# Optimization experiments

Measured on AMD Instinct MI355X. Metric: run time of the kernel, lower is better.

Reference implementation:

```python
import jax, jax.numpy as jnp
import numpy as np

B, C_IN, N, K, UP = 8, 128, 2048, 8, 4
C_MID = C_IN + 3  # 131

def _pw1(x, W):  # pointwise Conv1d: x (B,C,N), W (O,C)
    return jnp.einsum('oc,bcn->bon', W, x)

def _pw2(x, W):  # pointwise Conv2d: x (B,C,N,K), W (O,C)
    return jnp.einsum('oc,bcnk->bonk', W, x)

def _bn(x, g, b):  # eval-mode BatchNorm (running mean 0, var 1)
    shp = (1, -1) + (1,) * (x.ndim - 2)
    return x * g.reshape(shp) + b.reshape(shp)

def _gather(tab, idx):  # tab (B,S,D), idx (B,...) -> (B,...,D)
    return jax.vmap(lambda t, i: t[i])(tab, idx)

def _fps(pts, npoint):  # pts (B,n,c) -> idx (B,npoint), iterative farthest point sampling
    b, n, _ = pts.shape
    dist0 = jnp.full((b, n), 1e10, pts.dtype)
    far0 = jnp.zeros((b,), jnp.int32)
    def body(carry, _):
        dist, far = carry
        cen = jax.vmap(lambda p, i: p[i])(pts, far)[:, None, :]  # (b,1,c)
        d = jnp.sum((pts - cen) ** 2, axis=-1)
        dist = jnp.minimum(dist, d)
        return (dist, jnp.argmax(dist, axis=-1).astype(jnp.int32)), far
    (_, _), idx = jax.lax.scan(body, (dist0, far0), None, length=npoint)
    return idx.T  # (B, npoint)

def _forward(feature, input, rel_pos_emb, w_skip, g_skip, b_skip, w_m1, w_m2, g_m2, b_m2,
             w_out1, g_out1, b_out1, w_out2, g_out2, b_out2, w_q, w_k, w_v, b_v,
             w_t, b_t, g_ra, b_ra, w_mlp1, w_conv2, g_conv2, b_conv2):
    b, c, n = feature.shape
    s = n // UP
    pts = feature.reshape(b, n, c)  # mirrors torch .reshape(B,N,C)
    far = _fps(pts, s)                          # (B,S) FPS in feature space
    down_feats = _gather(pts, far)              # (B,S,C) downsampled features
    xyz = jnp.transpose(input, (0, 2, 1))       # (B,N,3)
    cand_xyz = _gather(xyz, far)                # (B,S,3)
    # kNN: each of N input points -> k nearest downsampled points (xyz space)
    d2 = (jnp.sum(xyz ** 2, -1)[:, :, None] + jnp.sum(cand_xyz ** 2, -1)[:, None, :]
          - 2.0 * jnp.einsum('bnd,bsd->bns', xyz, cand_xyz))
    _, idx = jax.lax.top_k(-d2, K)              # (B,N,K)
    gp = jnp.transpose(_gather(cand_xyz, idx), (0, 3, 1, 2))    # (B,3,N,K)
    gf = jnp.transpose(_gather(down_feats, idx), (0, 3, 1, 2))  # (B,C,N,K)
    gp = gp - input[:, :, :, None]              # relative coords
    feats = jnp.concatenate([gf, gp], axis=1)   # (B,131,N,K)
    skip = jnp.max(feats, axis=3)
    skip = jax.nn.relu(_bn(_pw1(skip, w_skip), g_skip, b_skip))         # (B,256,N)
    f = jax.nn.relu(_pw2(feats, w_m1))
    f = jax.nn.relu(_bn(_pw2(f, w_m2), g_m2, b_m2))                     # (B,256,N,K)
    # output_mlp1: Conv2d(k->256, kernel [1,256]) on f.transpose(1,3)
    g1 = jnp.einsum('okw,bwnk->bon', w_out1, f)                         # (B,256,N)
    g1 = jax.nn.relu(_bn(g1, g_out1, b_out1))
    g1 = g1 + skip
    g1 = jax.nn.relu(_bn(_pw1(g1, w_out2), g_out2, b_out2))             # (B,128,N)
    glob = jnp.concatenate([g1, input], axis=1)                          # (B,131,N)
    # RA_Layer1: PCT-style offset attention
    q = jnp.transpose(_pw1(glob, w_q), (0, 2, 1))                        # (B,N,32)
    kk = _pw1(glob, w_k)                                                 # (B,32,N)
    v = _pw1(glob, w_v) + b_v[None, :, None]
    att = jax.nn.softmax(jnp.einsum('bnc,bcm->bnm', q, kk), axis=-1)     # (B,N,N)
    att = att / (1e-9 + att.sum(axis=1, keepdims=True))
    x_r = jnp.einsum('bcm,bmn->bcn', v, att)
    x_r = jax.nn.relu(_bn(_pw1(glob - x_r, w_t) + b_t[None, :, None], g_ra, b_ra))
    ra = glob + x_r
    out = jax.nn.relu(_pw1(ra, w_mlp1))                                  # (B,256,N)
    out = jax.nn.relu(_bn(_pw1(out, w_conv2), g_conv2, b_conv2))         # (B,128,N)
    return out

def setup_inputs():
    key = jax.random.key(0)
    ks = iter(jax.random.split(key, 40))
    def nrm(shape, scale=1.0):
        return jax.random.normal(next(ks), shape, jnp.float32) * scale
    return {
        'feature': nrm((B, C_IN, N)),
        'input': nrm((B, 3, N)),
        'rel_pos_emb': nrm((B, 3, N)),
        'w_skip': nrm((256, C_MID), 0.05), 'g_skip': jnp.ones((256,)), 'b_skip': jnp.zeros((256,)),
        'w_m1': nrm((256, C_MID), 0.05),
        'w_m2': nrm((256, 256), 0.05), 'g_m2': jnp.ones((256,)), 'b_m2': jnp.zeros((256,)),
        'w_out1': nrm((256, K, 256), 0.02), 'g_out1': jnp.ones((256,)), 'b_out1': jnp.zeros((256,)),
        'w_out2': nrm((128, 256), 0.05), 'g_out2': jnp.ones((128,)), 'b_out2': jnp.zeros((128,)),
        'w_q': nrm((C_MID // 4, C_MID), 0.05), 'w_k': nrm((C_MID // 4, C_MID), 0.05),
        'w_v': nrm((C_MID, C_MID), 0.05), 'b_v': jnp.zeros((C_MID,)),
        'w_t': nrm((C_MID, C_MID), 0.05), 'b_t': jnp.zeros((C_MID,)),
        'g_ra': jnp.ones((C_MID,)), 'b_ra': jnp.zeros((C_MID,)),
        'w_mlp1': nrm((256, C_MID), 0.05),
        'w_conv2': nrm((128, 256), 0.05), 'g_conv2': jnp.ones((128,)), 'b_conv2': jnp.zeros((128,)),
    }

def reference(feature, input, rel_pos_emb, w_skip, g_skip, b_skip, w_m1, w_m2, g_m2, b_m2,
              w_out1, g_out1, b_out1, w_out2, g_out2, b_out2, w_q, w_k, w_v, b_v,
              w_t, b_t, g_ra, b_ra, w_mlp1, w_conv2, g_conv2, b_conv2):
    return _forward(feature, input, rel_pos_emb, w_skip, g_skip, b_skip, w_m1, w_m2, g_m2, b_m2,
                    w_out1, g_out1, b_out1, w_out2, g_out2, b_out2, w_q, w_k, w_v, b_v,
                    w_t, b_t, g_ra, b_ra, w_mlp1, w_conv2, g_conv2, b_conv2)
```

## Files before the change

kernel.cpp:

```cpp
#include <hip/hip_runtime.h>


#define NB 8
#define NN 2048
#define CIN 128
#define KNN 8
#define SS 512
#define CMID 131

enum { F_XT = 1, F_STORET = 4, F_XSUB = 8 };

template <int FLAGS>
__global__ __launch_bounds__(256) void gemm64_k(
    const float* __restrict__ W, size_t wbs,
    const float* __restrict__ X, size_t xbs,
    const float* __restrict__ X2,
    float* __restrict__ Y, size_t ybs, int ldyt,
    int O, int K, int M,
    const float* __restrict__ bias,
    const float* __restrict__ gamma,
    const float* __restrict__ beta,
    const float* __restrict__ skip, size_t skipbs,
    const float* __restrict__ colscale,
    int relu)
{
    constexpr int KC = 32;
    __shared__ float Wl[KC * 68];
    __shared__ float Xl[KC * 68];
    const int b  = blockIdx.z;
    const int o0 = blockIdx.y * 64, m0 = blockIdx.x * 64;
    const float* Wb  = W + (size_t)b * wbs;
    const float* Xb  = X + (size_t)b * xbs;
    const float* X2b = (FLAGS & F_XSUB) ? (X2 + (size_t)b * xbs) : nullptr;
    const int t  = threadIdx.x;
    const int to = t >> 4, tm = t & 15;
    const int o4 = to * 4, m4 = tm * 4;

    float acc[4][4];
#pragma unroll
    for (int i = 0; i < 4; ++i)
#pragma unroll
        for (int j = 0; j < 4; ++j) acc[i][j] = 0.f;

    for (int kk = 0; kk < K; kk += KC) {
#pragma unroll
        for (int r = 0; r < 8; ++r) {
            int e = t + r * 256;
            int ki = e & 31, o = e >> 5;
            int go = o0 + o, gk = kk + ki;
            Wl[ki * 68 + o] = (go < O && gk < K) ? Wb[(size_t)go * K + gk] : 0.f;
        }
        if (FLAGS & F_XT) {
#pragma unroll
            for (int r = 0; r < 8; ++r) {
                int e = t + r * 256;
                int ki = e & 31, m = e >> 5;
                int gm = m0 + m, gk = kk + ki;
                Xl[ki * 68 + m] = (gm < M && gk < K) ? Xb[(size_t)gm * K + gk] : 0.f;
            }
        } else {
#pragma unroll
            for (int r = 0; r < 2; ++r) {
                int e = t + r * 256;
                int kr = e >> 4, mc4 = (e & 15) * 4;
                int gk = kk + kr;
                float4 v = make_float4(0.f, 0.f, 0.f, 0.f);
                if (gk < K) {
                    v = *(const float4*)&Xb[(size_t)gk * M + m0 + mc4];
                    if (FLAGS & F_XSUB) {
                        float4 u = *(const float4*)&X2b[(size_t)gk * M + m0 + mc4];
                        v.x -= u.x; v.y -= u.y; v.z -= u.z; v.w -= u.w;
                    }
                }
                *(float4*)&Xl[kr * 68 + mc4] = v;
            }
        }
        __syncthreads();
#pragma unroll
        for (int k = 0; k < KC; ++k) {
            float4 w4 = *(const float4*)&Wl[k * 68 + o4];
            float4 x4 = *(const float4*)&Xl[k * 68 + m4];
            float wv[4] = {w4.x, w4.y, w4.z, w4.w};
            float xv[4] = {x4.x, x4.y, x4.z, x4.w};
#pragma unroll
            for (int i = 0; i < 4; ++i)
#pragma unroll
                for (int j = 0; j < 4; ++j)
                    acc[i][j] = fmaf(wv[i], xv[j], acc[i][j]);
        }
        __syncthreads();
    }
#pragma unroll
    for (int i = 0; i < 4; ++i) {
        int o = o0 + o4 + i;
        if (o >= O) continue;
        float bi_ = bias ? bias[o] : 0.f;
        float ga  = gamma ? gamma[o] : 1.f;
        float be  = gamma ? beta[o] : 0.f;
        float v4[4];
#pragma unroll
        for (int j = 0; j < 4; ++j) {
            int m = m0 + m4 + j;
            float v = acc[i][j] + bi_;
            v = v * ga + be;
            if (relu) v = fmaxf(v, 0.f);
            if (skip) v += skip[(size_t)b * skipbs + (size_t)o * M + m];
            if (colscale) v *= colscale[(size_t)b * M + m];
            v4[j] = v;
        }
        if (FLAGS & F_STORET) {
#pragma unroll
            for (int j = 0; j < 4; ++j)
                Y[(size_t)b * ybs + (size_t)(m0 + m4 + j) * ldyt + o] = v4[j];
        } else {
            float4 s = make_float4(v4[0], v4[1], v4[2], v4[3]);
            *(float4*)&Y[(size_t)b * ybs + (size_t)o * M + m0 + m4] = s;
        }
    }
}

__global__ __launch_bounds__(256) void fps_k(const float* __restrict__ G,
                                             int* __restrict__ far)
{
    const int b = blockIdx.x;
    const float* Gb = G + (size_t)b * NN * NN;
    const int t = threadIdx.x;
    const int pA = 4 * t, pB = 1024 + 4 * t;

    float4 dstA = make_float4(1e10f, 1e10f, 1e10f, 1e10f);
    float4 dstB = dstA;
    float4 dgA, dgB;
    dgA.x = Gb[(size_t)(pA + 0) * NN + (pA + 0)];
    dgA.y = Gb[(size_t)(pA + 1) * NN + (pA + 1)];
    dgA.z = Gb[(size_t)(pA + 2) * NN + (pA + 2)];
    dgA.w = Gb[(size_t)(pA + 3) * NN + (pA + 3)];
    dgB.x = Gb[(size_t)(pB + 0) * NN + (pB + 0)];
    dgB.y = Gb[(size_t)(pB + 1) * NN + (pB + 1)];
    dgB.z = Gb[(size_t)(pB + 2) * NN + (pB + 2)];
    dgB.w = Gb[(size_t)(pB + 3) * NN + (pB + 3)];

    __shared__ float sv[2][4];
    __shared__ int   si[2][4];
    int cur = 0;
    if (t == 0) far[b * SS] = 0;

    for (int it = 1; it < SS; ++it) {
        const float* row = Gb + (size_t)cur * NN;
        float nf = row[cur];
        float4 rA = *(const float4*)&row[pA];
        float4 rB = *(const float4*)&row[pB];

        dstA.x = fminf(dstA.x, dgA.x + nf - 2.0f * rA.x);
        dstA.y = fminf(dstA.y, dgA.y + nf - 2.0f * rA.y);
        dstA.z = fminf(dstA.z, dgA.z + nf - 2.0f * rA.z);
        dstA.w = fminf(dstA.w, dgA.w + nf - 2.0f * rA.w);
        dstB.x = fminf(dstB.x, dgB.x + nf - 2.0f * rB.x);
        dstB.y = fminf(dstB.y, dgB.y + nf - 2.0f * rB.y);
        dstB.z = fminf(dstB.z, dgB.z + nf - 2.0f * rB.z);
        dstB.w = fminf(dstB.w, dgB.w + nf - 2.0f * rB.w);

        float best = dstA.x; int bidx = pA;
        if (dstA.y > best) { best = dstA.y; bidx = pA + 1; }
        if (dstA.z > best) { best = dstA.z; bidx = pA + 2; }
        if (dstA.w > best) { best = dstA.w; bidx = pA + 3; }
        if (dstB.x > best) { best = dstB.x; bidx = pB; }
        if (dstB.y > best) { best = dstB.y; bidx = pB + 1; }
        if (dstB.z > best) { best = dstB.z; bidx = pB + 2; }
        if (dstB.w > best) { best = dstB.w; bidx = pB + 3; }

#pragma unroll
        for (int off = 32; off >= 1; off >>= 1) {
            float ov = __shfl_xor(best, off, 64);
            int   oi = __shfl_xor(bidx, off, 64);
            if (ov > best || (ov == best && oi < bidx)) { best = ov; bidx = oi; }
        }
        const int wid = t >> 6, lane = t & 63, pb = it & 1;
        if (lane == 0) { sv[pb][wid] = best; si[pb][wid] = bidx; }
        __syncthreads();
        float bb = sv[pb][0]; int bi_ = si[pb][0];
#pragma unroll
        for (int w = 1; w < 4; ++w) {
            float wv = sv[pb][w]; int wi = si[pb][w];
            if (wv > bb || (wv == bb && wi < bi_)) { bb = wv; bi_ = wi; }
        }
        cur = bi_;
        if (t == 0) far[b * SS + it] = bi_;
    }
}

__global__ __launch_bounds__(256) void gather_df_k(const float* __restrict__ feature,
                                                   const int* __restrict__ far,
                                                   float* __restrict__ dcT)
{
    int idx = blockIdx.x * 256 + threadIdx.x;
    int c = idx & 127;
    int s = (idx >> 7) & 511;
    int b = idx >> 16;
    float v = feature[(size_t)b * (NN * CIN) + (size_t)far[b * SS + s] * CIN + c];
    dcT[((size_t)b * CMID + c) * SS + s] = v;
}

__global__ void gather_cx_k(const float* __restrict__ input,
                            const int* __restrict__ far,
                            float* __restrict__ cand,
                            float* __restrict__ dcT)
{
    int idx = blockIdx.x * 64 + threadIdx.x;
    if (idx >= NB * SS) return;
    int b = idx >> 9, s = idx & 511;
    int f = far[idx];
#pragma unroll
    for (int d = 0; d < 3; ++d) {
        float v = input[((size_t)b * 3 + d) * NN + f];
        cand[idx * 3 + d] = v;
        dcT[((size_t)b * CMID + CIN + d) * SS + s] = v;
    }
}

__global__ __launch_bounds__(256) void b1_k(const float* __restrict__ W1,
                                            const float* __restrict__ input,
                                            float* __restrict__ B1)
{
    const int b = blockIdx.y;
    const int t = threadIdx.x;
    const int n = blockIdx.x * 4 + (t >> 6);
    const int w4 = (t & 63) * 4;
    float in0 = input[(size_t)b * (3 * NN) + n];
    float in1 = input[(size_t)b * (3 * NN) + NN + n];
    float in2 = input[(size_t)b * (3 * NN) + 2 * NN + n];
    float4 v;
    float* vp = &v.x;
#pragma unroll
    for (int j = 0; j < 4; ++j) {
        const float* wr = &W1[(size_t)(w4 + j) * CMID + CIN];
        vp[j] = wr[0] * in0 + wr[1] * in1 + wr[2] * in2;
    }
    *(float4*)&B1[((size_t)b * NN + n) * 256 + w4] = v;
}

__global__ __launch_bounds__(256) void w2t_k(const float* __restrict__ W2,
                                             float* __restrict__ W2T)
{
    int idx = blockIdx.x * 256 + threadIdx.x;
    int w = idx >> 8, v = idx & 255;
    W2T[(size_t)v * 256 + w] = W2[(size_t)w * 256 + v];
}

__global__ __launch_bounds__(256) void wot_k(const float* __restrict__ WO,
                                             float* __restrict__ WOT)
{
    int idx = blockIdx.x * 256 + threadIdx.x;
    int w = idx & 255, ko = idx >> 8;
    int o = ko & 255, k = ko >> 8;
    WOT[((size_t)k * 256 + w) * 256 + o] = WO[((size_t)o * 8 + k) * 256 + w];
}

__global__ __launch_bounds__(256) void knn_k(const float* __restrict__ input,
                                             const float* __restrict__ cand,
                                             int* __restrict__ kidx)
{
    __shared__ float cx[SS], cy[SS], cz[SS], cn2[SS];
    int b = blockIdx.y;
    int t = threadIdx.x;
#pragma unroll
    for (int r = 0; r < 2; ++r) {
        int s = t + r * 256;
        float x = cand[(b * SS + s) * 3 + 0];
        float y = cand[(b * SS + s) * 3 + 1];
        float z = cand[(b * SS + s) * 3 + 2];
        cx[s] = x; cy[s] = y; cz[s] = z;
        cn2[s] = x * x + y * y + z * z;
    }
    __syncthreads();
    int n = blockIdx.x * 256 + t;
    float px = input[(size_t)b * (3 * NN) + n];
    float py = input[(size_t)b * (3 * NN) + NN + n];
    float pz = input[(size_t)b * (3 * NN) + 2 * NN + n];
    float pn2 = px * px + py * py + pz * pz;
    float bd[8]; int bi[8];
#pragma unroll
    for (int i = 0; i < 8; ++i) { bd[i] = 1e30f; bi[i] = 0; }
    for (int s = 0; s < SS; ++s) {
        float d = pn2 + cn2[s] - 2.f * (px * cx[s] + py * cy[s] + pz * cz[s]);
        if (d < bd[7]) {
            float v = d; int vi = s;
#pragma unroll
            for (int p = 0; p < 8; ++p) {
                bool sw = v < bd[p];
                float tv = sw ? bd[p] : v;
                int   ti = sw ? bi[p] : vi;
                if (sw) { bd[p] = v; bi[p] = vi; }
                v = tv; vi = ti;
            }
        }
    }
#pragma unroll
    for (int k = 0; k < 8; ++k)
        kidx[((size_t)b * NN + n) * 8 + k] = bi[k];
}

__global__ __launch_bounds__(256) void skipfeat_k(const float* __restrict__ dcT,
                                                  const float* __restrict__ input,
                                                  const int* __restrict__ kidx,
                                                  float* __restrict__ sk)
{
    int b = blockIdx.z, c = blockIdx.y;
    int n = blockIdx.x * 256 + threadIdx.x;
    const int* kp = &kidx[((size_t)b * NN + n) * 8];
    int id[8];
#pragma unroll
    for (int k = 0; k < 8; ++k) id[k] = kp[k];
    const float* row = &dcT[((size_t)b * CMID + c) * SS];
    float m;
    if (c < CIN) {
        m = row[id[0]];
#pragma unroll
        for (int k = 1; k < 8; ++k) m = fmaxf(m, row[id[k]]);
    } else {
        float x = input[(size_t)b * (3 * NN) + (size_t)(c - CIN) * NN + n];
        m = row[id[0]] - x;
#pragma unroll
        for (int k = 1; k < 8; ++k) m = fmaxf(m, row[id[k]] - x);
    }
    sk[((size_t)b * CMID + c) * NN + n] = m;
}

__global__ __launch_bounds__(256) void mlp2_k(
    const float* __restrict__ A1, const float* __restrict__ B1,
    const int* __restrict__ kidx,
    const float* __restrict__ W2T, const float* __restrict__ WOT,
    const float* __restrict__ g2v, const float* __restrict__ b2v,
    float* __restrict__ pgbuf)
{
    __shared__ float fL[256 * 36];
    __shared__ int klAll[4][32];
    const int b = blockIdx.z;
    const int half = blockIdx.y;
    const int n0 = blockIdx.x * 32;
    const int t = threadIdx.x;
    const float* A1b = A1 + (size_t)b * (SS * 256);
    const float* B1b = B1 + (size_t)b * ((size_t)NN * 256);

    if (t < 128) {
        int k = t >> 5, n = t & 31;
        klAll[k][n] = kidx[((size_t)b * NN + n0 + n) * 8 + (half * 4 + k)];
    }
    const int to = t >> 3, tm = t & 7;
    const int ob = to * 8, nb = tm * 4;
    const int gn = t & 31, gg = t >> 5;

    float pg[8][4];
#pragma unroll
    for (int i = 0; i < 8; ++i)
#pragma unroll
        for (int j = 0; j < 4; ++j) pg[i][j] = 0.f;

#pragma unroll 1
    for (int k = 0; k < 4; ++k) {
        __syncthreads();
        {
            int id = klAll[k][gn];
            const float* arow = &A1b[(size_t)id * 256];
            const float* brow = &B1b[(size_t)(n0 + gn) * 256];
#pragma unroll
            for (int r = 0; r < 8; ++r) {
                int w4 = (gg + r * 8) * 4;
                float4 a = *(const float4*)&arow[w4];
                float4 bb = *(const float4*)&brow[w4];
                fL[(w4 + 0) * 36 + gn] = fmaxf(a.x - bb.x, 0.f);
                fL[(w4 + 1) * 36 + gn] = fmaxf(a.y - bb.y, 0.f);
                fL[(w4 + 2) * 36 + gn] = fmaxf(a.z - bb.z, 0.f);
                fL[(w4 + 3) * 36 + gn] = fmaxf(a.w - bb.w, 0.f);
            }
        }
        __syncthreads();
        float acc[8][4];
#pragma unroll
        for (int i = 0; i < 8; ++i)
#pragma unroll
            for (int j = 0; j < 4; ++j) acc[i][j] = 0.f;
#pragma unroll 4
        for (int ki = 0; ki < 256; ++ki) {
            float4 x4 = *(const float4*)&fL[ki * 36 + nb];
            float4 w0 = *(const float4*)&W2T[(size_t)ki * 256 + ob];
            float4 w1 = *(const float4*)&W2T[(size_t)ki * 256 + ob + 4];
            float wa[8] = {w0.x, w0.y, w0.z, w0.w, w1.x, w1.y, w1.z, w1.w};
            float xa[4] = {x4.x, x4.y, x4.z, x4.w};
#pragma unroll
            for (int i = 0; i < 8; ++i)
#pragma unroll
                for (int j = 0; j < 4; ++j)
                    acc[i][j] = fmaf(wa[i], xa[j], acc[i][j]);
        }
        __syncthreads();
#pragma unroll
        for (int i = 0; i < 8; ++i) {
            int o = ob + i;
            float ga = g2v[o], be = b2v[o];
            float4 v;
            v.x = fmaxf(fmaf(acc[i][0], ga, be), 0.f);
            v.y = fmaxf(fmaf(acc[i][1], ga, be), 0.f);
            v.z = fmaxf(fmaf(acc[i][2], ga, be), 0.f);
            v.w = fmaxf(fmaf(acc[i][3], ga, be), 0.f);
            *(float4*)&fL[(size_t)(ob + i) * 36 + nb] = v;
        }
        __syncthreads();
        const float* WOTk = &WOT[(size_t)(half * 4 + k) * 256 * 256];
#pragma unroll 4
        for (int ki = 0; ki < 256; ++ki) {
            float4 x4 = *(const float4*)&fL[ki * 36 + nb];
            float4 w0 = *(const float4*)&WOTk[(size_t)ki * 256 + ob];
            float4 w1 = *(const float4*)&WOTk[(size_t)ki * 256 + ob + 4];
            float wa[8] = {w0.x, w0.y, w0.z, w0.w, w1.x, w1.y, w1.z, w1.w};
            float xa[4] = {x4.x, x4.y, x4.z, x4.w};
#pragma unroll
            for (int i = 0; i < 8; ++i)
#pragma unroll
                for (int j = 0; j < 4; ++j)
                    pg[i][j] = fmaf(wa[i], xa[j], pg[i][j]);
        }
    }
#pragma unroll
    for (int i = 0; i < 8; ++i) {
        size_t base = (((size_t)(half * NB + b)) * 256 + (ob + i)) * NN + n0 + nb;
        float4 v = make_float4(pg[i][0], pg[i][1], pg[i][2], pg[i][3]);
        *(float4*)&pgbuf[base] = v;
    }
}

__global__ __launch_bounds__(256) void g1fin_k(const float* __restrict__ pgbuf,
                                               const float* __restrict__ g3v,
                                               const float* __restrict__ b3v,
                                               const float* __restrict__ skip2,
                                               float* __restrict__ g1)
{
    const size_t HALF = (size_t)NB * 256 * NN / 4;
    size_t idx = (size_t)blockIdx.x * 256 + threadIdx.x;
    int o = (int)((idx / (NN / 4)) & 255);
    float4 p0 = ((const float4*)pgbuf)[idx];
    float4 p1 = ((const float4*)pgbuf)[idx + HALF];
    float4 sk = ((const float4*)skip2)[idx];
    float ga = g3v[o], be = b3v[o];
    float4 v;
    v.x = fmaxf(fmaf(p0.x + p1.x, ga, be), 0.f) + sk.x;
    v.y = fmaxf(fmaf(p0.y + p1.y, ga, be), 0.f) + sk.y;
    v.z = fmaxf(fmaf(p0.z + p1.z, ga, be), 0.f) + sk.z;
    v.w = fmaxf(fmaf(p0.w + p1.w, ga, be), 0.f) + sk.w;
    ((float4*)g1)[idx] = v;
}

__global__ void globin_k(const float* __restrict__ input, float* __restrict__ glob)
{
    int idx = blockIdx.x * 256 + threadIdx.x;
    int b = idx / (3 * NN), rem = idx % (3 * NN);
    glob[(size_t)b * (CMID * NN) + (size_t)(CIN * NN) + rem] = input[idx];
}

__global__ __launch_bounds__(256) void softmax_k(float* __restrict__ att)
{
    int b = blockIdx.y;
    float4* row = (float4*)(att + ((size_t)b * NN + blockIdx.x) * NN);
    int t = threadIdx.x;
    float4 a = row[t], c = row[t + 256];
    float m = fmaxf(fmaxf(fmaxf(a.x, a.y), fmaxf(a.z, a.w)),
                    fmaxf(fmaxf(c.x, c.y), fmaxf(c.z, c.w)));
#pragma unroll
    for (int off = 32; off >= 1; off >>= 1) m = fmaxf(m, __shfl_xor(m, off, 64));
    __shared__ float sh[4];
    int wid = t >> 6, lane = t & 63;
    if (lane == 0) sh[wid] = m;
    __syncthreads();
    m = fmaxf(fmaxf(sh[0], sh[1]), fmaxf(sh[2], sh[3]));
    a.x = expf(a.x - m); a.y = expf(a.y - m); a.z = expf(a.z - m); a.w = expf(a.w - m);
    c.x = expf(c.x - m); c.y = expf(c.y - m); c.z = expf(c.z - m); c.w = expf(c.w - m);
    float s = a.x + a.y + a.z + a.w + c.x + c.y + c.z + c.w;
#pragma unroll
    for (int off = 32; off >= 1; off >>= 1) s += __shfl_xor(s, off, 64);
    __syncthreads();
    if (lane == 0) sh[wid] = s;
    __syncthreads();
    s = sh[0] + sh[1] + sh[2] + sh[3];
    float inv = 1.f / s;
    a.x *= inv; a.y *= inv; a.z *= inv; a.w *= inv;
    c.x *= inv; c.y *= inv; c.z *= inv; c.w *= inv;
    row[t] = a; row[t + 256] = c;
}

__global__ __launch_bounds__(256) void colsum_part_k(const float* __restrict__ att,
                                                     float* __restrict__ part)
{
    int j = blockIdx.x * 256 + threadIdx.x;
    int rc = blockIdx.y, b = blockIdx.z;
    const float* p = att + (size_t)b * NN * NN + (size_t)rc * 256 * NN + j;
    float s = 0.f;
    for (int i = 0; i < 256; ++i) s += p[(size_t)i * NN];
    part[((size_t)b * 8 + rc) * NN + j] = s;
}

__global__ __launch_bounds__(256) void colsum_fin_k(const float* __restrict__ part,
                                                    float* __restrict__ inv)
{
    int j = blockIdx.x * 256 + threadIdx.x;
    int b = blockIdx.y;
    float s = 0.f;
#pragma unroll
    for (int r = 0; r < 8; ++r) s += part[((size_t)b * 8 + r) * NN + j];
    inv[b * NN + j] = 1.f / (1e-9f + s);
}

extern "C" void kernel_launch(void* const* d_in, const int* in_sizes, int n_in,
                              void* d_out, int out_size, void* d_ws, size_t ws_size,
                              hipStream_t stream)
{
    (void)in_sizes; (void)n_in; (void)out_size;
    const float* feature = (const float*)d_in[0];
    const float* input   = (const float*)d_in[1];
    const float* w_skip  = (const float*)d_in[3];
    const float* g_skip  = (const float*)d_in[4];
    const float* b_skip  = (const float*)d_in[5];
    const float* w_m1    = (const float*)d_in[6];
    const float* w_m2    = (const float*)d_in[7];
    const float* g_m2    = (const float*)d_in[8];
    const float* b_m2    = (const float*)d_in[9];
    const float* w_out1  = (const float*)d_in[10];
    const float* g_out1  = (const float*)d_in[11];
    const float* b_out1  = (const float*)d_in[12];
    const float* w_out2  = (const float*)d_in[13];
    const float* g_out2  = (const float*)d_in[14];
    const float* b_out2  = (const float*)d_in[15];
    const float* w_q     = (const float*)d_in[16];
    const float* w_k     = (const float*)d_in[17];
    const float* w_v     = (const float*)d_in[18];
    const float* b_v     = (const float*)d_in[19];
    const float* w_t     = (const float*)d_in[20];
    const float* b_t     = (const float*)d_in[21];
    const float* g_ra    = (const float*)d_in[22];
    const float* b_ra    = (const float*)d_in[23];
    const float* w_mlp1  = (const float*)d_in[24];
    const float* w_conv2 = (const float*)d_in[25];
    const float* g_conv2 = (const float*)d_in[26];
    const float* b_conv2 = (const float*)d_in[27];
    float* out = (float*)d_out;
    float* ws  = (float*)d_ws;

    if (ws_size < (size_t)52932608 * 4) return;

    float* G     = ws;
    float* att   = ws;
    float* pgbuf = ws;
    float* B1    = ws + 29360128;
    int*   far   = (int*)(ws + 33554432);
    float* dcT   = ws + 33558528;
    float* cand  = ws + 34095104;
    int*   kidx  = (int*)(ws + 34107392);
    float* A1    = ws + 34238464;
    float* skmax = ws + 35287040;
    float* skip2 = ws + 37433344;
    float* g1    = ws + 41627648;
    float* glob  = ws + 45821952;
    float* q_t   = ws + 47968256;
    float* kkb   = ws + 48492544;
    float* vb    = ws + 49016832;
    float* ics   = ws + 51163136;
    float* csp   = ws + 51179520;
    float* W2T   = ws + 51310592;
    float* WOT   = ws + 51376128;
    float* ra    = skmax;
    float* mid   = skip2;
    float* x_r   = g1;

    const size_t GLB = (size_t)CMID * NN;

    gemm64_k<F_XT><<<dim3(32, 32, NB), 256, 0, stream>>>(
        feature, (size_t)NN * CIN, feature, (size_t)NN * CIN, nullptr,
        G, (size_t)NN * NN, 0, NN, CIN, NN,
        nullptr, nullptr, nullptr, nullptr, 0, nullptr, 0);
    fps_k<<<NB, 256, 0, stream>>>(G, far);
    gather_df_k<<<(NB * SS * CIN) / 256, 256, 0, stream>>>(feature, far, dcT);
    gather_cx_k<<<(NB * SS) / 64, 64, 0, stream>>>(input, far, cand, dcT);
    b1_k<<<dim3(NN / 4, NB), 256, 0, stream>>>(w_m1, input, B1);
    w2t_k<<<256, 256, 0, stream>>>(w_m2, W2T);
    wot_k<<<2048, 256, 0, stream>>>(w_out1, WOT);
    knn_k<<<dim3(NN / 256, NB), 256, 0, stream>>>(input, cand, kidx);
    skipfeat_k<<<dim3(NN / 256, CMID, NB), 256, 0, stream>>>(dcT, input, kidx, skmax);
    gemm64_k<0><<<dim3(32, 4, NB), 256, 0, stream>>>(
        w_skip, 0, skmax, GLB, nullptr, skip2, (size_t)256 * NN, 0,
        256, CMID, NN, nullptr, g_skip, b_skip, nullptr, 0, nullptr, 1);
    gemm64_k<F_STORET><<<dim3(8, 4, NB), 256, 0, stream>>>(
        w_m1, 0, dcT, (size_t)CMID * SS, nullptr, A1, (size_t)SS * 256, 256,
        256, CMID, SS, nullptr, nullptr, nullptr, nullptr, 0, nullptr, 0);
    mlp2_k<<<dim3(NN / 32, 2, NB), 256, 0, stream>>>(
        A1, B1, kidx, W2T, WOT, g_m2, b_m2, pgbuf);
    g1fin_k<<<(NB * 256 * NN / 4) / 256, 256, 0, stream>>>(
        pgbuf, g_out1, b_out1, skip2, g1);
    gemm64_k<0><<<dim3(32, 2, NB), 256, 0, stream>>>(
        w_out2, 0, g1, (size_t)256 * NN, nullptr, glob, GLB, 0,
        128, 256, NN, nullptr, g_out2, b_out2, nullptr, 0, nullptr, 1);
    globin_k<<<(NB * 3 * NN) / 256, 256, 0, stream>>>(input, glob);
    gemm64_k<F_STORET><<<dim3(32, 1, NB), 256, 0, stream>>>(
        w_q, 0, glob, GLB, nullptr, q_t, (size_t)NN * 32, 32,
        32, CMID, NN, nullptr, nullptr, nullptr, nullptr, 0, nullptr, 0);
    gemm64_k<0><<<dim3(32, 1, NB), 256, 0, stream>>>(
        w_k, 0, glob, GLB, nullptr, kkb, (size_t)32 * NN, 0,
        32, CMID, NN, nullptr, nullptr, nullptr, nullptr, 0, nullptr, 0);
    gemm64_k<0><<<dim3(32, 3, NB), 256, 0, stream>>>(
        w_v, 0, glob, GLB, nullptr, vb, GLB, 0,
        CMID, CMID, NN, b_v, nullptr, nullptr, nullptr, 0, nullptr, 0);
    gemm64_k<0><<<dim3(32, 32, NB), 256, 0, stream>>>(
        q_t, (size_t)NN * 32, kkb, (size_t)32 * NN, nullptr, att, (size_t)NN * NN, 0,
        NN, 32, NN, nullptr, nullptr, nullptr, nullptr, 0, nullptr, 0);
    softmax_k<<<dim3(NN, NB), 256, 0, stream>>>(att);
    colsum_part_k<<<dim3(NN / 256, 8, NB), 256, 0, stream>>>(att, csp);
    colsum_fin_k<<<dim3(NN / 256, NB), 256, 0, stream>>>(csp, ics);
    gemm64_k<0><<<dim3(32, 3, NB), 256, 0, stream>>>(
        vb, GLB, att, (size_t)NN * NN, nullptr, x_r, GLB, 0,
        CMID, NN, NN, nullptr, nullptr, nullptr, nullptr, 0, ics, 0);
    gemm64_k<F_XSUB><<<dim3(32, 3, NB), 256, 0, stream>>>(
        w_t, 0, glob, GLB, x_r, ra, GLB, 0,
        CMID, CMID, NN, b_t, g_ra, b_ra, glob, GLB, nullptr, 1);
    gemm64_k<0><<<dim3(32, 4, NB), 256, 0, stream>>>(
        w_mlp1, 0, ra, GLB, nullptr, mid, (size_t)256 * NN, 0,
        256, CMID, NN, nullptr, nullptr, nullptr, nullptr, 0, nullptr, 1);
    gemm64_k<0><<<dim3(32, 2, NB), 256, 0, stream>>>(
        w_conv2, 0, mid, (size_t)256 * NN, nullptr, out, (size_t)128 * NN, 0,
        128, 256, NN, nullptr, g_conv2, b_conv2, nullptr, 0, nullptr, 1);
}
```

Before: 2.339 ms.

## Add 128x128 register-tiled GEMM and widen mlp2 tile to 64 points

Adds a gemm128 kernel where each thread computes an 8x8 output tile from 128x128 block tiles with a K chunk of 32. Most pointwise GEMMs, including the Gram matrix and the attention GEMMs, now use it instead of the 64-tile kernel. The fused mlp2 kernel now processes 64 points per block with 8x8 per-thread accumulators. The aim is more arithmetic per shared-memory and global load and fewer reloads of the weight matrices, at the cost of more registers and shared memory per block, fewer blocks, and padding waste for O=131.

```diff
diff --git a/kernel.cpp b/kernel.cpp
--- a/kernel.cpp
+++ b/kernel.cpp
@@ -119,6 +119,112 @@
     }
 }
 
+template <int FLAGS>
+__global__ __launch_bounds__(256) void gemm128_k(
+    const float* __restrict__ W, size_t wbs,
+    const float* __restrict__ X, size_t xbs,
+    const float* __restrict__ X2,
+    float* __restrict__ Y, size_t ybs,
+    int O, int K, int M,
+    const float* __restrict__ bias,
+    const float* __restrict__ gamma,
+    const float* __restrict__ beta,
+    const float* __restrict__ skip, size_t skipbs,
+    const float* __restrict__ colscale,
+    int relu)
+{
+    constexpr int KC = 32;
+    __shared__ float Wl[KC * 132];
+    __shared__ float Xl[KC * 132];
+    const int b  = blockIdx.z;
+    const int o0 = blockIdx.y * 128, m0 = blockIdx.x * 128;
+    const float* Wb  = W + (size_t)b * wbs;
+    const float* Xb  = X + (size_t)b * xbs;
+    const float* X2b = (FLAGS & F_XSUB) ? (X2 + (size_t)b * xbs) : nullptr;
+    const int t   = threadIdx.x;
+    const int to4 = (t >> 4) * 4;
+    const int tm4 = (t & 15) * 4;
+
+    float acc[8][8];
+#pragma unroll
+    for (int i = 0; i < 8; ++i)
+#pragma unroll
+        for (int j = 0; j < 8; ++j) acc[i][j] = 0.f;
+
+    for (int kk = 0; kk < K; kk += KC) {
+#pragma unroll
+        for (int r = 0; r < 16; ++r) {
+            int e = t + r * 256;
+            int ki = e & 31, o = e >> 5;
+            int go = o0 + o, gk = kk + ki;
+            Wl[ki * 132 + o] = (go < O && gk < K) ? Wb[(size_t)go * K + gk] : 0.f;
+        }
+        if (FLAGS & F_XT) {
+#pragma unroll
+            for (int r = 0; r < 16; ++r) {
+                int e = t + r * 256;
+                int ki = e & 31, m = e >> 5;
+                int gm = m0 + m, gk = kk + ki;
+                Xl[ki * 132 + m] = (gm < M && gk < K) ? Xb[(size_t)gm * K + gk] : 0.f;
+            }
+        } else {
+#pragma unroll
+            for (int r = 0; r < 4; ++r) {
+                int e = t + r * 256;
+                int kr = e >> 5, mc4 = (e & 31) * 4;
+                int gk = kk + kr;
+                float4 v = make_float4(0.f, 0.f, 0.f, 0.f);
+                if (gk < K) {
+                    v = *(const float4*)&Xb[(size_t)gk * M + m0 + mc4];
+                    if (FLAGS & F_XSUB) {
+                        float4 u = *(const float4*)&X2b[(size_t)gk * M + m0 + mc4];
+                        v.x -= u.x; v.y -= u.y; v.z -= u.z; v.w -= u.w;
+                    }
+                }
+                *(float4*)&Xl[kr * 132 + mc4] = v;
+            }
+        }
+        __syncthreads();
+#pragma unroll 4
+        for (int ki = 0; ki < KC; ++ki) {
+            float4 w0 = *(const float4*)&Wl[ki * 132 + to4];
+            float4 w1 = *(const float4*)&Wl[ki * 132 + 64 + to4];
+            float4 x0 = *(const float4*)&Xl[ki * 132 + tm4];
+            float4 x1 = *(const float4*)&Xl[ki * 132 + 64 + tm4];
+            float wa[8] = {w0.x, w0.y, w0.z, w0.w, w1.x, w1.y, w1.z, w1.w};
+            float xa[8] = {x0.x, x0.y, x0.z, x0.w, x1.x, x1.y, x1.z, x1.w};
+#pragma unroll
+            for (int i = 0; i < 8; ++i)
+#pragma unroll
+                for (int j = 0; j < 8; ++j)
+                    acc[i][j] = fmaf(wa[i], xa[j], acc[i][j]);
+        }
+        __syncthreads();
+    }
+#pragma unroll
+    for (int i = 0; i < 8; ++i) {
+        int o = o0 + ((i >> 2) * 64) + to4 + (i & 3);
+        if (o >= O) continue;
+        float bi_ = bias ? bias[o] : 0.f;
+        float ga  = gamma ? gamma[o] : 1.f;
+        float be  = gamma ? beta[o] : 0.f;
+        float v[8];
+#pragma unroll
+        for (int j = 0; j < 8; ++j) {
+            int m = m0 + ((j >> 2) * 64) + tm4 + (j & 3);
+            float x = acc[i][j] + bi_;
+            x = x * ga + be;
+            if (relu) x = fmaxf(x, 0.f);
+            if (skip) x += skip[(size_t)b * skipbs + (size_t)o * M + m];
+            if (colscale) x *= colscale[(size_t)b * M + m];
+            v[j] = x;
+        }
+        size_t base = (size_t)b * ybs + (size_t)o * M + m0;
+        *(float4*)&Y[base + tm4]      = make_float4(v[0], v[1], v[2], v[3]);
+        *(float4*)&Y[base + 64 + tm4] = make_float4(v[4], v[5], v[6], v[7]);
+    }
+}
+
 __global__ __launch_bounds__(256) void fps_k(const float* __restrict__ G,
                                              int* __restrict__ far)
 {
@@ -332,28 +438,28 @@
     const float* __restrict__ g2v, const float* __restrict__ b2v,
     float* __restrict__ pgbuf)
 {
-    __shared__ float fL[256 * 36];
-    __shared__ int klAll[4][32];
+    __shared__ float fL[256 * 72];
+    __shared__ int klAll[4][64];
     const int b = blockIdx.z;
     const int half = blockIdx.y;
-    const int n0 = blockIdx.x * 32;
+    const int n0 = blockIdx.x * 64;
     const int t = threadIdx.x;
     const float* A1b = A1 + (size_t)b * (SS * 256);
     const float* B1b = B1 + (size_t)b * ((size_t)NN * 256);
 
-    if (t < 128) {
-        int k = t >> 5, n = t & 31;
+    {
+        int k = t >> 6, n = t & 63;
         klAll[k][n] = kidx[((size_t)b * NN + n0 + n) * 8 + (half * 4 + k)];
     }
-    const int to = t >> 3, tm = t & 7;
-    const int ob = to * 8, nb = tm * 4;
-    const int gn = t & 31, gg = t >> 5;
-
-    float pg[8][4];
+    const int to4 = (t >> 3) * 4;
+    const int tm4 = (t & 7) * 4;
+    const int gn = t & 63, gg = t >> 6;
+
+    float pg[8][8];
 #pragma unroll
     for (int i = 0; i < 8; ++i)
 #pragma unroll
-        for (int j = 0; j < 4; ++j) pg[i][j] = 0.f;
+        for (int j = 0; j < 8; ++j) pg[i][j] = 0.f;
 
 #pragma unroll 1
     for (int k = 0; k < 4; ++k) {
@@ -363,68 +469,75 @@
             const float* arow = &A1b[(size_t)id * 256];
             const float* brow = &B1b[(size_t)(n0 + gn) * 256];
 #pragma unroll
-            for (int r = 0; r < 8; ++r) {
-                int w4 = (gg + r * 8) * 4;
+            for (int r = 0; r < 16; ++r) {
+                int w4 = (gg + r * 4) * 4;
                 float4 a = *(const float4*)&arow[w4];
                 float4 bb = *(const float4*)&brow[w4];
-                fL[(w4 + 0) * 36 + gn] = fmaxf(a.x - bb.x, 0.f);
-                fL[(w4 + 1) * 36 + gn] = fmaxf(a.y - bb.y, 0.f);
-                fL[(w4 + 2) * 36 + gn] = fmaxf(a.z - bb.z, 0.f);
-                fL[(w4 + 3) * 36 + gn] = fmaxf(a.w - bb.w, 0.f);
+                fL[(w4 + 0) * 72 + gn] = fmaxf(a.x - bb.x, 0.f);
+                fL[(w4 + 1) * 72 + gn] = fmaxf(a.y - bb.y, 0.f);
+                fL[(w4 + 2) * 72 + gn] = fmaxf(a.z - bb.z, 0.f);
+                fL[(w4 + 3) * 72 + gn] = fmaxf(a.w - bb.w, 0.f);
             }
         }
         __syncthreads();
-        float acc[8][4];
+        float acc[8][8];
 #pragma unroll
         for (int i = 0; i < 8; ++i)
 #pragma unroll
-            for (int j = 0; j < 4; ++j) acc[i][j] = 0.f;
-#pragma unroll 4
+            for (int j = 0; j < 8; ++j) acc[i][j] = 0.f;
+#pragma unroll 2
         for (int ki = 0; ki < 256; ++ki) {
-            float4 x4 = *(const float4*)&fL[ki * 36 + nb];
-            float4 w0 = *(const float4*)&W2T[(size_t)ki * 256 + ob];
-            float4 w1 = *(const float4*)&W2T[(size_t)ki * 256 + ob + 4];
+            float4 x0 = *(const float4*)&fL[ki * 72 + tm4];
+            float4 x1 = *(const float4*)&fL[ki * 72 + 32 + tm4];
+            float4 w0 = *(const float4*)&W2T[(size_t)ki * 256 + to4];
+            float4 w1 = *(const float4*)&W2T[(size_t)ki * 256 + 128 + to4];
             float wa[8] = {w0.x, w0.y, w0.z, w0.w, w1.x, w1.y, w1.z, w1.w};
-            float xa[4] = {x4.x, x4.y, x4.z, x4.w};
+            float xa[8] = {x0.x, x0.y, x0.z, x0.w, x1.x, x1.y, x1.z, x1.w};
 #pragma unroll
             for (int i = 0; i < 8; ++i)
 #pragma unroll
-                for (int j = 0; j < 4; ++j)
+                for (int j = 0; j < 8; ++j)
                     acc[i][j] = fmaf(wa[i], xa[j], acc[i][j]);
         }
         __syncthreads();
 #pragma unroll
         for (int i = 0; i < 8; ++i) {
-            int o = ob + i;
+            int o = ((i >> 2) * 128) + to4 + (i & 3);
             float ga = g2v[o], be = b2v[o];
-            float4 v;
-            v.x = fmaxf(fmaf(acc[i][0], ga, be), 0.f);
-            v.y = fmaxf(fmaf(acc[i][1], ga, be), 0.f);
-            v.z = fmaxf(fmaf(acc[i][2], ga, be), 0.f);
-            v.w = fmaxf(fmaf(acc[i][3], ga, be), 0.f);
-            *(float4*)&fL[(size_t)(ob + i) * 36 + nb] = v;
+            float v0 = fmaxf(fmaf(acc[i][0], ga, be), 0.f);
+            float v1 = fmaxf(fmaf(acc[i][1], ga, be), 0.f);
+            float v2 = fmaxf(fmaf(acc[i][2], ga, be), 0.f);
+            float v3 = fmaxf(fmaf(acc[i][3], ga, be), 0.f);
+            float v4 = fmaxf(fmaf(acc[i][4], ga, be), 0.f);
+            float v5 = fmaxf(fmaf(acc[i][5], ga, be), 0.f);
+            float v6 = fmaxf(fmaf(acc[i][6], ga, be), 0.f);
+            float v7 = fmaxf(fmaf(acc[i][7], ga, be), 0.f);
+            *(float4*)&fL[(size_t)o * 72 + tm4]      = make_float4(v0, v1, v2, v3);
+            *(float4*)&fL[(size_t)o * 72 + 32 + tm4] = make_float4(v4, v5, v6, v7);
         }
         __syncthreads();
         const float* WOTk = &WOT[(size_t)(half * 4 + k) * 256 * 256];
-#pragma unroll 4
+#pragma unroll 2
         for (int ki = 0; ki < 256; ++ki) {
-            float4 x4 = *(const float4*)&fL[ki * 36 + nb];
-            float4 w0 = *(const float4*)&WOTk[(size_t)ki * 256 + ob];
-            float4 w1 = *(const float4*)&WOTk[(size_t)ki * 256 + ob + 4];
+            float4 x0 = *(const float4*)&fL[ki * 72 + tm4];
+            float4 x1 = *(const float4*)&fL[ki * 72 + 32 + tm4];
+            float4 w0 = *(const float4*)&WOTk[(size_t)ki * 256 + to4];
+            float4 w1 = *(const float4*)&WOTk[(size_t)ki * 256 + 128 + to4];
             float wa[8] = {w0.x, w0.y, w0.z, w0.w, w1.x, w1.y, w1.z, w1.w};
-            float xa[4] = {x4.x, x4.y, x4.z, x4.w};
+            float xa[8] = {x0.x, x0.y, x0.z, x0.w, x1.x, x1.y, x1.z, x1.w};
 #pragma unroll
             for (int i = 0; i < 8; ++i)
 #pragma unroll
-                for (int j = 0; j < 4; ++j)
+                for (int j = 0; j < 8; ++j)
                     pg[i][j] = fmaf(wa[i], xa[j], pg[i][j]);
         }
     }
 #pragma unroll
     for (int i = 0; i < 8; ++i) {
-        size_t base = (((size_t)(half * NB + b)) * 256 + (ob + i)) * NN + n0 + nb;
-        float4 v = make_float4(pg[i][0], pg[i][1], pg[i][2], pg[i][3]);
-        *(float4*)&pgbuf[base] = v;
+        int o = ((i >> 2) * 128) + to4 + (i & 3);
+        size_t base = (((size_t)(half * NB + b)) * 256 + o) * NN + n0;
+        *(float4*)&pgbuf[base + tm4]      = make_float4(pg[i][0], pg[i][1], pg[i][2], pg[i][3]);
+        *(float4*)&pgbuf[base + 32 + tm4] = make_float4(pg[i][4], pg[i][5], pg[i][6], pg[i][7]);
     }
 }
 
@@ -571,9 +684,9 @@
 
     const size_t GLB = (size_t)CMID * NN;
 
-    gemm64_k<F_XT><<<dim3(32, 32, NB), 256, 0, stream>>>(
+    gemm128_k<F_XT><<<dim3(16, 16, NB), 256, 0, stream>>>(
         feature, (size_t)NN * CIN, feature, (size_t)NN * CIN, nullptr,
-        G, (size_t)NN * NN, 0, NN, CIN, NN,
+        G, (size_t)NN * NN, NN, CIN, NN,
         nullptr, nullptr, nullptr, nullptr, 0, nullptr, 0);
     fps_k<<<NB, 256, 0, stream>>>(G, far);
     gather_df_k<<<(NB * SS * CIN) / 256, 256, 0, stream>>>(feature, far, dcT);
@@ -583,18 +696,18 @@
     wot_k<<<2048, 256, 0, stream>>>(w_out1, WOT);
     knn_k<<<dim3(NN / 256, NB), 256, 0, stream>>>(input, cand, kidx);
     skipfeat_k<<<dim3(NN / 256, CMID, NB), 256, 0, stream>>>(dcT, input, kidx, skmax);
-    gemm64_k<0><<<dim3(32, 4, NB), 256, 0, stream>>>(
-        w_skip, 0, skmax, GLB, nullptr, skip2, (size_t)256 * NN, 0,
+    gemm128_k<0><<<dim3(16, 2, NB), 256, 0, stream>>>(
+        w_skip, 0, skmax, GLB, nullptr, skip2, (size_t)256 * NN,
         256, CMID, NN, nullptr, g_skip, b_skip, nullptr, 0, nullptr, 1);
     gemm64_k<F_STORET><<<dim3(8, 4, NB), 256, 0, stream>>>(
         w_m1, 0, dcT, (size_t)CMID * SS, nullptr, A1, (size_t)SS * 256, 256,
         256, CMID, SS, nullptr, nullptr, nullptr, nullptr, 0, nullptr, 0);
-    mlp2_k<<<dim3(NN / 32, 2, NB), 256, 0, stream>>>(
+    mlp2_k<<<dim3(NN / 64, 2, NB), 256, 0, stream>>>(
         A1, B1, kidx, W2T, WOT, g_m2, b_m2, pgbuf);
     g1fin_k<<<(NB * 256 * NN / 4) / 256, 256, 0, stream>>>(
         pgbuf, g_out1, b_out1, skip2, g1);
-    gemm64_k<0><<<dim3(32, 2, NB), 256, 0, stream>>>(
-        w_out2, 0, g1, (size_t)256 * NN, nullptr, glob, GLB, 0,
+    gemm128_k<0><<<dim3(16, 1, NB), 256, 0, stream>>>(
+        w_out2, 0, g1, (size_t)256 * NN, nullptr, glob, GLB,
         128, 256, NN, nullptr, g_out2, b_out2, nullptr, 0, nullptr, 1);
     globin_k<<<(NB * 3 * NN) / 256, 256, 0, stream>>>(input, glob);
     gemm64_k<F_STORET><<<dim3(32, 1, NB), 256, 0, stream>>>(
@@ -603,25 +716,25 @@
     gemm64_k<0><<<dim3(32, 1, NB), 256, 0, stream>>>(
         w_k, 0, glob, GLB, nullptr, kkb, (size_t)32 * NN, 0,
         32, CMID, NN, nullptr, nullptr, nullptr, nullptr, 0, nullptr, 0);
-    gemm64_k<0><<<dim3(32, 3, NB), 256, 0, stream>>>(
-        w_v, 0, glob, GLB, nullptr, vb, GLB, 0,
+    gemm128_k<0><<<dim3(16, 2, NB), 256, 0, stream>>>(
+        w_v, 0, glob, GLB, nullptr, vb, GLB,
         CMID, CMID, NN, b_v, nullptr, nullptr, nullptr, 0, nullptr, 0);
-    gemm64_k<0><<<dim3(32, 32, NB), 256, 0, stream>>>(
-        q_t, (size_t)NN * 32, kkb, (size_t)32 * NN, nullptr, att, (size_t)NN * NN, 0,
+    gemm128_k<0><<<dim3(16, 16, NB), 256, 0, stream>>>(
+        q_t, (size_t)NN * 32, kkb, (size_t)32 * NN, nullptr, att, (size_t)NN * NN,
         NN, 32, NN, nullptr, nullptr, nullptr, nullptr, 0, nullptr, 0);
     softmax_k<<<dim3(NN, NB), 256, 0, stream>>>(att);
     colsum_part_k<<<dim3(NN / 256, 8, NB), 256, 0, stream>>>(att, csp);
     colsum_fin_k<<<dim3(NN / 256, NB), 256, 0, stream>>>(csp, ics);
-    gemm64_k<0><<<dim3(32, 3, NB), 256, 0, stream>>>(
-        vb, GLB, att, (size_t)NN * NN, nullptr, x_r, GLB, 0,
+    gemm128_k<0><<<dim3(16, 2, NB), 256, 0, stream>>>(
+        vb, GLB, att, (size_t)NN * NN, nullptr, x_r, GLB,
         CMID, NN, NN, nullptr, nullptr, nullptr, nullptr, 0, ics, 0);
-    gemm64_k<F_XSUB><<<dim3(32, 3, NB), 256, 0, stream>>>(
-        w_t, 0, glob, GLB, x_r, ra, GLB, 0,
+    gemm128_k<F_XSUB><<<dim3(16, 2, NB), 256, 0, stream>>>(
+        w_t, 0, glob, GLB, x_r, ra, GLB,
         CMID, CMID, NN, b_t, g_ra, b_ra, glob, GLB, nullptr, 1);
-    gemm64_k<0><<<dim3(32, 4, NB), 256, 0, stream>>>(
-        w_mlp1, 0, ra, GLB, nullptr, mid, (size_t)256 * NN, 0,
+    gemm128_k<0><<<dim3(16, 2, NB), 256, 0, stream>>>(
+        w_mlp1, 0, ra, GLB, nullptr, mid, (size_t)256 * NN,
         256, CMID, NN, nullptr, nullptr, nullptr, nullptr, 0, nullptr, 1);
-    gemm64_k<0><<<dim3(32, 2, NB), 256, 0, stream>>>(
-        w_conv2, 0, mid, (size_t)256 * NN, nullptr, out, (size_t)128 * NN, 0,
+    gemm128_k<0><<<dim3(16, 1, NB), 256, 0, stream>>>(
+        w_conv2, 0, mid, (size_t)256 * NN, nullptr, out, (size_t)128 * NN,
         128, 256, NN, nullptr, g_conv2, b_conv2, nullptr, 0, nullptr, 1);
 }
```

Measured after the change: 3.058 ms. 1.31x slower.
